# Optimization experiments

Measured on AMD Instinct MI355X. Metric: run time of the kernel, lower is better.

The kernel has to match this reference:

```python
import jax, jax.numpy as jnp
import numpy as np

# --- constants mirroring init_kwargs ---
DIM = 1024
N_HEADS = 16
N_KV_HEADS = 4
HEAD_DIM = DIM // N_HEADS          # 64
REP = N_HEADS // N_KV_HEADS        # 4
ROPE_THETA = 10000.0
WINDOW = 512
N_GLOBAL = 64
EPS = 1e-6


def setup_inputs() -> dict:
    key = jax.random.key(0)
    ks = jax.random.split(key, 7)
    B, L = 2, 2048
    x = jax.random.normal(ks[0], (B, L, DIM), dtype=jnp.float32)
    s = 0.02
    wq = jax.random.normal(ks[1], (DIM, N_HEADS * HEAD_DIM), dtype=jnp.float32) * s
    wk = jax.random.normal(ks[2], (DIM, N_KV_HEADS * HEAD_DIM), dtype=jnp.float32) * s
    wv = jax.random.normal(ks[3], (DIM, N_KV_HEADS * HEAD_DIM), dtype=jnp.float32) * s
    wo = jax.random.normal(ks[4], (N_HEADS * HEAD_DIM, DIM), dtype=jnp.float32) * s
    gq = jnp.ones((HEAD_DIM,), dtype=jnp.float32) + 0.01 * jax.random.normal(ks[5], (HEAD_DIM,), dtype=jnp.float32)
    gk = jnp.ones((HEAD_DIM,), dtype=jnp.float32) + 0.01 * jax.random.normal(ks[6], (HEAD_DIM,), dtype=jnp.float32)
    return {"x": x, "wq": wq, "wk": wk, "wv": wv, "wo": wo, "gq": gq, "gk": gk}


def _rmsnorm(t, g):
    # QKNorm: RMS norm over head_dim with learnable per-dim scale
    return t * jax.lax.rsqrt(jnp.mean(t * t, axis=-1, keepdims=True) + EPS) * g


def _rope(t, cos, sin):
    # t: [B,H,L,hd]; complex RoPE over consecutive pairs (2i, 2i+1)
    t1 = t[..., 0::2]
    t2 = t[..., 1::2]
    o1 = t1 * cos - t2 * sin
    o2 = t1 * sin + t2 * cos
    return jnp.stack([o1, o2], axis=-1).reshape(t.shape)


def reference(x, wq, wk, wv, wo, gq, gk):
    B, L, D = x.shape
    q = (x @ wq).reshape(B, L, N_HEADS, HEAD_DIM)
    k = (x @ wk).reshape(B, L, N_KV_HEADS, HEAD_DIM)
    v = (x @ wv).reshape(B, L, N_KV_HEADS, HEAD_DIM)
    q = _rmsnorm(q, gq)
    k = _rmsnorm(k, gk)
    q = q.transpose(0, 2, 1, 3)  # [B,H,L,hd]
    k = k.transpose(0, 2, 1, 3)
    v = v.transpose(0, 2, 1, 3)

    # RoPE frequencies (start_pos = 0)
    inv_freq = 1.0 / (ROPE_THETA ** (jnp.arange(0, HEAD_DIM, 2, dtype=jnp.float32) / HEAD_DIM))
    ang = jnp.arange(L, dtype=jnp.float32)[:, None] * inv_freq[None, :]  # [L, hd/2]
    cos, sin = jnp.cos(ang), jnp.sin(ang)
    q = _rope(q, cos, sin)
    k = _rope(k, cos, sin)

    # GQA: repeat kv heads (repeat_interleave on head dim)
    k = jnp.repeat(k, REP, axis=1)
    v = jnp.repeat(v, REP, axis=1)

    scores = jnp.einsum("bhqd,bhkd->bhqk", q, k) / np.sqrt(HEAD_DIM).astype(np.float32)

    # sliding-window + global-token causal mask
    half = WINDOW // 2
    i = jnp.arange(L)[:, None]
    j = jnp.arange(L)[None, :]
    m = (j <= i) & ((j >= i - half) | (j < N_GLOBAL))  # [L,L] bool
    scores = jnp.where(m[None, None], scores, -jnp.inf)

    attn = jax.nn.softmax(scores.astype(jnp.float32), axis=-1).astype(scores.dtype)
    out = jnp.einsum("bhqk,bhkd->bhqd", attn, v)
    out = out.transpose(0, 2, 1, 3).reshape(B, L, N_HEADS * HEAD_DIM)
    return out @ wo
```

## Files before the change

kernel.cpp:

```cpp
#include <hip/hip_runtime.h>
#include <hip/hip_bf16.h>

typedef __bf16 bf16x8 __attribute__((ext_vector_type(8)));
typedef __bf16 bf16x4 __attribute__((ext_vector_type(4)));
typedef float  f32x4  __attribute__((ext_vector_type(4)));
typedef short  s16x4  __attribute__((ext_vector_type(4)));

__device__ __forceinline__ __bf16 to_bf16(float f) {
    __hip_bfloat16 h = __float2bfloat16(f);
    return *reinterpret_cast<__bf16*>(&h);
}

__device__ __forceinline__ f32x4 mfma32(bf16x8 a, bf16x8 b, f32x4 c) {
    return __builtin_amdgcn_mfma_f32_16x16x32_bf16(a, b, c, 0, 0, 0);
}
__device__ __forceinline__ f32x4 mfma16(bf16x4 a, bf16x4 b, f32x4 c) {
#if __has_builtin(__builtin_amdgcn_mfma_f32_16x16x16_bf16)
    return __builtin_amdgcn_mfma_f32_16x16x16_bf16(a, b, c, 0, 0, 0);
#else
    return __builtin_amdgcn_mfma_f32_16x16x16bf16_1k(
        __builtin_bit_cast(s16x4, a), __builtin_bit_cast(s16x4, b), c, 0, 0, 0);
#endif
}

__device__ __forceinline__ void gload_lds16(const __bf16* g, __bf16* l) {
    __builtin_amdgcn_global_load_lds(
        (const __attribute__((address_space(1))) void*)g,
        (__attribute__((address_space(3))) void*)l, 16, 0, 0);
}


__global__ __launch_bounds__(256) void prep_k(const float* __restrict__ wq,
                                              const float* __restrict__ wk,
                                              const float* __restrict__ wv,
                                              __bf16* __restrict__ WqkvT,
                                              float2* __restrict__ rope_tab) {
    int b = blockIdx.x, tid = threadIdx.x;
    if (b >= 1536) {
        int idx = (b - 1536) * 256 + tid;
        int pos = idx >> 5, f = idx & 31;
        float ex = (float)(2 * f) * (1.0f / 64.0f);
        float invf = expf(-ex * 9.210340371976184f);
        float ang = (float)pos * invf;
        rope_tab[idx] = make_float2(cosf(ang), sinf(ang));
        return;
    }
    __shared__ float tile[32][36];
    const float* src; __bf16* dst; int N, idx;
    if (b < 1024)      { src = wq; dst = WqkvT;                        N = 1024; idx = b; }
    else if (b < 1280) { src = wk; dst = WqkvT + (size_t)1024 * 1024;  N = 256;  idx = b - 1024; }
    else               { src = wv; dst = WqkvT + (size_t)1280 * 1024;  N = 256;  idx = b - 1280; }
    int k0 = (idx & 31) * 32, n0 = (idx >> 5) * 32;
    int row = tid >> 3, c4 = tid & 7;
    *(f32x4*)&tile[row][c4 * 4] = *(const f32x4*)(src + (size_t)(k0 + row) * N + n0 + c4 * 4);
    __syncthreads();
    bf16x4 v;
#pragma unroll
    for (int j = 0; j < 4; ++j) v[j] = to_bf16(tile[c4 * 4 + j][row]);
    *(bf16x4*)&dst[(size_t)(n0 + row) * 1024 + k0 + c4 * 4] = v;
}

__global__ __launch_bounds__(512, 4) void gemmqkv_k(const float* __restrict__ X,
                                                    const __bf16* __restrict__ BT,
                                                    const float2* __restrict__ rope_tab,
                                                    const float* __restrict__ gq,
                                                    const float* __restrict__ gk,
                                                    const float* __restrict__ wo,
                                                    __bf16* __restrict__ Qb,
                                                    __bf16* __restrict__ Kbl,
                                                    __bf16* __restrict__ Vt,
                                                    __bf16* __restrict__ WoT) {
    extern __shared__ char smem_raw[];
    if (blockIdx.y >= 12) {
        float* scr = (float*)smem_raw;
        int bidT = (blockIdx.y - 12) * 32 + blockIdx.x;
        int sub = threadIdx.x >> 8, t8 = threadIdx.x & 255;
        int row = t8 >> 3, c4 = t8 & 7;
        float* my = scr + sub * 1152;
#pragma unroll
        for (int r = 0; r < 4; ++r) {
            int tile = bidT * 8 + r * 2 + sub;
            int k0 = (tile & 31) * 32, n0t = (tile >> 5) * 32;
            __syncthreads();
            *(f32x4*)&my[row * 36 + c4 * 4] =
                *(const f32x4*)(wo + (size_t)(k0 + row) * 1024 + n0t + c4 * 4);
            __syncthreads();
            bf16x4 v;
#pragma unroll
            for (int j = 0; j < 4; ++j) v[j] = to_bf16(my[(c4 * 4 + j) * 36 + row]);
            *(bf16x4*)&WoT[(size_t)(n0t + row) * 1024 + k0 + c4 * 4] = v;
        }
        return;
    }
    __shared__ float ssp[4][128];
    __bf16* smem = (__bf16*)smem_raw;
    int tid = threadIdx.x;
    int m0 = blockIdx.x * 128, n0 = blockIdx.y * 128;
    int wid = tid >> 6, lane = tid & 63;
    int wm = (wid & 1) * 64, wn = (wid >> 1) * 32;
    int lm = lane & 15, qd = lane >> 4;
    int srow = tid >> 2, sc4 = tid & 3;
    int ac16 = (tid & 3) * 16;
    int akh = ac16 >> 5, ac4 = (ac16 & 31) >> 3;
    f32x4 acc[4][2] = {};
    f32x4 areg[4];

    auto A_LOAD = [&](int t) {
        const float* ap = X + (size_t)(m0 + srow) * 1024 + t * 64 + ac16;
        areg[0] = *(const f32x4*)(ap);
        areg[1] = *(const f32x4*)(ap + 4);
        areg[2] = *(const f32x4*)(ap + 8);
        areg[3] = *(const f32x4*)(ap + 12);
    };
    auto A_WRITE = [&](int bsel) {
        __bf16* base = smem + bsel * 16384 + akh * 4096 + srow * 32;
        bf16x8 w0, w1;
#pragma unroll
        for (int j = 0; j < 4; ++j) {
            w0[j] = to_bf16(areg[0][j]); w0[4 + j] = to_bf16(areg[1][j]);
            w1[j] = to_bf16(areg[2][j]); w1[4 + j] = to_bf16(areg[3][j]);
        }
        *(bf16x8*)&base[ac4 * 8] = w0;
        *(bf16x8*)&base[(ac4 + 1) * 8] = w1;
    };
    auto B_GLOAD = [&](int bsel, int t) {
        __bf16* base = smem + bsel * 16384 + 8192;
#pragma unroll
        for (int kh = 0; kh < 2; ++kh)
            gload_lds16(BT + (size_t)(n0 + srow) * 1024 + t * 64 + kh * 32 + sc4 * 8,
                        base + kh * 4096 + wid * 512);
    };

    A_LOAD(0);
    B_GLOAD(0, 0);
    asm volatile("s_waitcnt vmcnt(2)" ::: "memory");
    A_WRITE(0);

    for (int t = 0; t < 16; ++t) {
        if (t + 1 < 16) {
            A_LOAD(t + 1);
            B_GLOAD((t + 1) & 1, t + 1);
            asm volatile("s_waitcnt vmcnt(6)" ::: "memory");
        } else {
            asm volatile("s_waitcnt vmcnt(0)" ::: "memory");
        }
        asm volatile("s_waitcnt lgkmcnt(0)" ::: "memory");
        __builtin_amdgcn_s_barrier();
        __builtin_amdgcn_sched_barrier(0);
        const __bf16* cA = smem + (t & 1) * 16384;
        const __bf16* cB = cA + 8192;
#pragma unroll
        for (int kh = 0; kh < 2; ++kh) {
            bf16x8 af[4], bfr[2];
#pragma unroll
            for (int t4 = 0; t4 < 4; ++t4) {
                int row = wm + t4 * 16 + lm;
                af[t4] = *(const bf16x8*)&cA[kh * 4096 + row * 32 + qd * 8];
            }
#pragma unroll
            for (int j = 0; j < 2; ++j) {
                int col = wn + j * 16 + lm;
                bfr[j] = *(const bf16x8*)&cB[kh * 4096 + col * 32 + qd * 8];
            }
#pragma unroll
            for (int ti = 0; ti < 4; ++ti)
#pragma unroll
                for (int tj = 0; tj < 2; ++tj)
                    acc[ti][tj] = mfma32(af[ti], bfr[tj], acc[ti][tj]);
        }
        if (t + 1 < 16) {
            asm volatile("s_waitcnt vmcnt(2)" ::: "memory");
            A_WRITE((t + 1) & 1);
        }
        asm volatile("s_waitcnt lgkmcnt(0)" ::: "memory");
        __builtin_amdgcn_s_barrier();
    }

    int head0 = n0 >> 6;
    int quad = wid >> 1;
    int chead = wn & 63;

    if (head0 < 20) {
        int head = head0 + (quad >> 1);
        bool isq = head < 16;
        const float* gvec = isq ? gq : gk;
        float gam[2];
#pragma unroll
        for (int tj = 0; tj < 2; ++tj) gam[tj] = gvec[chead + tj * 16 + lm];

#pragma unroll
        for (int ti = 0; ti < 4; ++ti)
#pragma unroll
            for (int r = 0; r < 4; ++r) {
                float sq = acc[ti][0][r] * acc[ti][0][r] + acc[ti][1][r] * acc[ti][1][r];
                sq += __shfl_xor(sq, 1);
                sq += __shfl_xor(sq, 2);
                sq += __shfl_xor(sq, 4);
                sq += __shfl_xor(sq, 8);
                if (lm == 0) ssp[quad][wm + ti * 16 + qd * 4 + r] = sq;
            }
        __syncthreads();

#pragma unroll
        for (int ti = 0; ti < 4; ++ti)
#pragma unroll
            for (int r = 0; r < 4; ++r) {
                int row = wm + ti * 16 + qd * 4 + r;
                int t = m0 + row;
                int pos = t & 2047, bb = t >> 11;
                float ss = ssp[quad][row] + ssp[quad ^ 1][row];
                float scale = rsqrtf(ss * (1.0f / 64.0f) + 1e-6f);
#pragma unroll
                for (int tj = 0; tj < 2; ++tj) {
                    int cw = chead + tj * 16 + lm;
                    float v = acc[ti][tj][r] * scale * gam[tj];
                    float2 cs = rope_tab[pos * 32 + (cw >> 1)];
                    float pv = __shfl_xor(v, 1);
                    float outv = (cw & 1) ? (pv * cs.y + v * cs.x) : (v * cs.x - pv * cs.y);
                    if (isq) {
                        int kvh = head >> 2, h4 = head & 3;
                        size_t off = (((((size_t)bb * 4 + kvh) * 128 + (pos >> 4)) * 4 + h4) * 16
                                      + (pos & 15)) * 64 + cw;
                        Qb[off] = to_bf16(outv * 0.125f);
                    } else {
                        int kvg = head - 16;
                        Kbl[(((size_t)bb * 4 + kvg) * 2048 + pos) * 64 + cw] = to_bf16(outv);
                    }
                }
            }
    } else {
        __bf16* tvh = smem + (quad >> 1) * 8704;
        int bb = m0 >> 11, pos0 = m0 & 2047;
#pragma unroll
        for (int ti = 0; ti < 4; ++ti)
#pragma unroll
            for (int tj = 0; tj < 2; ++tj)
#pragma unroll
                for (int r = 0; r < 4; ++r) {
                    int row = wm + ti * 16 + qd * 4 + r;
                    int cw = chead + tj * 16 + lm;
                    tvh[cw * 136 + row] = to_bf16(acc[ti][tj][r]);
                }
        __syncthreads();
        int hh = tid >> 8, t8 = tid & 255;
        int kvg = head0 + hh - 20;
        size_t gg = (size_t)bb * 4 + kvg;
        const __bf16* tvr = smem + hh * 8704;
#pragma unroll
        for (int p = 0; p < 4; ++p) {
            int d = p * 16 + (t8 >> 4);
            int tok = (t8 & 15) * 8;
            bf16x8 vvv = *(const bf16x8*)&tvr[d * 136 + tok];
            *(bf16x8*)(Vt + (gg * 64 + d) * 2048 + pos0 + tok) = vvv;
        }
    }
}

__global__ __launch_bounds__(512, 4) void gemm_op_k(const __bf16* __restrict__ A,
                                                    const __bf16* __restrict__ BT,
                                                    float* __restrict__ C) {
    extern __shared__ char smem_raw[];
    __bf16* smem = (__bf16*)smem_raw;
    int tid = threadIdx.x;
    int m0 = blockIdx.x * 128, n0 = blockIdx.y * 64;
    int wid = tid >> 6, lane = tid & 63;
    int wm = (wid & 3) * 32, wn = (wid >> 2) * 32;
    int lm = lane & 15, qd = lane >> 4;
    int srow = tid >> 2, sc4 = tid & 3;
    int bhalf = wid >> 2, bidx = tid & 255;
    int brow = bidx >> 2, bc4 = bidx & 3;
    f32x4 acc[2][2] = {};
    auto STAGE = [&](int bsel, int t) {
        __bf16* base = smem + bsel * 12288;
#pragma unroll
        for (int kh = 0; kh < 2; ++kh)
            gload_lds16(A + (size_t)(m0 + srow) * 1024 + t * 64 + kh * 32 + sc4 * 8,
                        base + kh * 4096 + wid * 512);
        gload_lds16(BT + (size_t)(n0 + brow) * 1024 + t * 64 + bhalf * 32 + bc4 * 8,
                    base + 8192 + bhalf * 2048 + (wid & 3) * 512);
    };
    STAGE(0, 0);
    for (int t = 0; t < 16; ++t) {
        if (t + 1 < 16) {
            STAGE((t + 1) & 1, t + 1);
            asm volatile("s_waitcnt vmcnt(3)" ::: "memory");
        } else {
            asm volatile("s_waitcnt vmcnt(0)" ::: "memory");
        }
        __builtin_amdgcn_s_barrier();
        __builtin_amdgcn_sched_barrier(0);
        const __bf16* cA = smem + (t & 1) * 12288;
        const __bf16* cB = cA + 8192;
#pragma unroll
        for (int kh = 0; kh < 2; ++kh) {
            bf16x8 af[2], bfr[2];
#pragma unroll
            for (int i = 0; i < 2; ++i) {
                int row = wm + i * 16 + lm;
                af[i] = *(const bf16x8*)&cA[kh * 4096 + row * 32 + qd * 8];
                int col = wn + i * 16 + lm;
                bfr[i] = *(const bf16x8*)&cB[kh * 2048 + col * 32 + qd * 8];
            }
#pragma unroll
            for (int ti = 0; ti < 2; ++ti)
#pragma unroll
                for (int tj = 0; tj < 2; ++tj)
                    acc[ti][tj] = mfma32(af[ti], bfr[tj], acc[ti][tj]);
        }
        asm volatile("s_waitcnt lgkmcnt(0)" ::: "memory");
        __builtin_amdgcn_s_barrier();
    }
#pragma unroll
    for (int ti = 0; ti < 2; ++ti)
#pragma unroll
        for (int tj = 0; tj < 2; ++tj)
#pragma unroll
            for (int r = 0; r < 4; ++r) {
                int row = m0 + wm + ti * 16 + qd * 4 + r;
                int col = n0 + wn + tj * 16 + lm;
                C[(size_t)row * 1024 + col] = acc[ti][tj][r];
            }
}

__global__ __launch_bounds__(512, 4) void attn_k(const __bf16* __restrict__ Qb,
                                                 const __bf16* __restrict__ Kbl,
                                                 const __bf16* __restrict__ Vt,
                                                 __bf16* __restrict__ aout) {
    __shared__ __bf16 Kt[2][64 * 64];
    __shared__ __bf16 Vl[2][64 * 64];
    int tid = threadIdx.x, wid = tid >> 6, lane = tid & 63;
    int l15 = lane & 15, quad = lane >> 4;
    int qb = blockIdx.x, kvh = blockIdx.y, b = blockIdx.z;
    int qg = wid >> 2;
    int h4 = wid & 3;
    int iw0 = qb * 32;
    int iw = iw0 + qg * 16;
    int g = b * 4 + kvh;
    int h = kvh * 4 + h4;
    int e7 = l15 & 7;

    int qbi = qb * 2 + qg;
    const __bf16* qp = Qb + ((((size_t)g * 128 + qbi) * 4 + h4) * 16 + l15) * 64 + quad * 8;
    bf16x8 qf0 = *(const bf16x8*)qp;
    bf16x8 qf1 = *(const bf16x8*)(qp + 32);

    int ts = (iw0 - 256) >> 6; if (ts < 1) ts = 1;
    int tmaxb = (iw0 + 31) >> 6;
    int n_all = (tmaxb >= ts) ? (tmaxb - ts + 2) : 1;
    int tmaxw = (iw + 15) >> 6;

    const __bf16* Kg = Kbl + (size_t)g * 2048 * 64;
    const __bf16* Vg = Vt + (size_t)g * 64 * 2048;

    int r0 = tid >> 3, c0 = tid & 7;
    int kl = r0 * 64 + ((c0 ^ (r0 & 7)) * 8);

    bf16x8 kr, vr;
    auto stage_load = [&](int tt) {
        kr = *(const bf16x8*)(Kg + (size_t)tt * 64 * 64 + r0 * 64 + c0 * 8);
        vr = *(const bf16x8*)(Vg + (size_t)r0 * 2048 + tt * 64 + c0 * 8);
    };
    auto stage_write = [&](int buf) {
        *(bf16x8*)&Kt[buf][kl] = kr;
        *(bf16x8*)&Vl[buf][kl] = vr;
    };

    stage_load(0);
    stage_write(0);

    f32x4 o[4] = {};
    float mr = -1e30f, lrp = 0.f;
    int iq = iw + l15;

    for (int idx = 0; idx < n_all; ++idx) {
        int tt = (idx == 0) ? 0 : ts + idx - 1;
        if (idx + 1 < n_all) stage_load(ts + idx);
        __syncthreads();
        int buf = idx & 1;

        f32x4 s[4] = {};
#pragma unroll
        for (int nt = 0; nt < 4; ++nt) {
            const __bf16* kp = &Kt[buf][(nt * 16 + l15) * 64];
            bf16x8 k0 = *(const bf16x8*)(kp + ((quad ^ e7) * 8));
            bf16x8 k1 = *(const bf16x8*)(kp + (((quad + 4) ^ e7) * 8));
            s[nt] = mfma32(k0, qf0, s[nt]);
            s[nt] = mfma32(k1, qf1, s[nt]);
        }

        bool need_mask = (tt >= tmaxw) || (tt >= 1 && tt * 64 < iw + 15 - 256);
        if (need_mask) {
#pragma unroll
            for (int nt = 0; nt < 4; ++nt)
#pragma unroll
                for (int r = 0; r < 4; ++r) {
                    int j = tt * 64 + nt * 16 + quad * 4 + r;
                    bool valid = (j <= iq) && ((j >= iq - 256) || (j < 64));
                    s[nt][r] = valid ? s[nt][r] : -1e30f;
                }
        }

        float mx = -1e30f;
#pragma unroll
        for (int nt = 0; nt < 4; ++nt)
#pragma unroll
            for (int r = 0; r < 4; ++r) mx = fmaxf(mx, s[nt][r]);
        mx = fmaxf(mx, __shfl_xor(mx, 16));
        mx = fmaxf(mx, __shfl_xor(mx, 32));
        float mn = fmaxf(mr, mx);
        float alpha = __expf(mr - mn);
        mr = mn;

        float ps = 0.f;
        bf16x4 pb[4];
#pragma unroll
        for (int nt = 0; nt < 4; ++nt)
#pragma unroll
            for (int r = 0; r < 4; ++r) {
                float pv = __expf(s[nt][r] - mn);
                ps += pv;
                pb[nt][r] = to_bf16(pv);
            }
        lrp = lrp * alpha + ps;

#pragma unroll
        for (int dt = 0; dt < 4; ++dt) {
            o[dt] *= alpha;
            const __bf16* vp = &Vl[buf][(dt * 16 + l15) * 64];
#pragma unroll
            for (int nt = 0; nt < 4; ++nt) {
                int c8 = 2 * nt + (quad >> 1);
                bf16x4 va = *(const bf16x4*)(vp + ((c8 ^ e7) * 8) + (quad & 1) * 4);
                o[dt] = mfma16(va, pb[nt], o[dt]);
            }
        }

        if (idx + 1 < n_all) stage_write((idx + 1) & 1);
    }

    lrp += __shfl_xor(lrp, 16);
    lrp += __shfl_xor(lrp, 32);
    float inv = 1.f / lrp;
    __syncthreads();
    __bf16* pr = (__bf16*)Kt + wid * 16 * 64;
#pragma unroll
    for (int dt = 0; dt < 4; ++dt)
#pragma unroll
        for (int r = 0; r < 4; ++r) {
            int e = dt * 16 + quad * 4 + r;
            int c8 = e >> 3;
            pr[l15 * 64 + ((c8 ^ e7) * 8) + (e & 7)] = to_bf16(o[dt][r] * inv);
        }
    bf16x8 o0 = *(const bf16x8*)(pr + l15 * 64 + (((2 * quad) ^ e7) * 8));
    bf16x8 o1 = *(const bf16x8*)(pr + l15 * 64 + (((2 * quad + 1) ^ e7) * 8));
    __bf16* op = aout + ((size_t)b * 2048 + iw + l15) * 1024 + h * 64 + quad * 16;
    *(bf16x8*)op = o0;
    *(bf16x8*)(op + 8) = o1;
}

extern "C" void kernel_launch(void* const* d_in, const int* in_sizes, int n_in,
                              void* d_out, int out_size, void* d_ws, size_t ws_size,
                              hipStream_t stream) {
    const float* x  = (const float*)d_in[0];
    const float* wq = (const float*)d_in[1];
    const float* wk = (const float*)d_in[2];
    const float* wv = (const float*)d_in[3];
    const float* wo = (const float*)d_in[4];
    const float* gq = (const float*)d_in[5];
    const float* gk = (const float*)d_in[6];
    float* out = (float*)d_out;

    char* ws = (char*)d_ws;
    __bf16*  WqkvT = (__bf16*)ws;
    __bf16*  WoT   = (__bf16*)(ws + 3145728);
    __bf16*  aout  = (__bf16*)(ws + 5242880);
    __bf16*  Kbl   = (__bf16*)(ws + 13631488);
    __bf16*  Vt    = (__bf16*)(ws + 15728640);
    __bf16*  Qb    = (__bf16*)(ws + 17825792);
    float2*  rtab  = (float2*)(ws + 26214400);

    prep_k<<<1792, dim3(256), 0, stream>>>(wq, wk, wv, WqkvT, rtab);
    gemmqkv_k<<<dim3(32, 16), dim3(512), 65536, stream>>>(x, WqkvT, rtab, gq, gk, wo,
                                                          Qb, Kbl, Vt, WoT);
    attn_k<<<dim3(64, 4, 2), dim3(512), 0, stream>>>(Qb, Kbl, Vt, aout);
    gemm_op_k<<<dim3(32, 16), dim3(512), 49152, stream>>>(aout, WoT, out);
}
```

Before: 142.1 us.

## Use 256-thread blocks with larger per-warp tiles in QKV and output GEMMs

Both GEMM kernels switch from 8 waves to 4 waves per block while keeping the same block tile, so each wave computes a bigger sub-tile (64x64 in QKV, 64x32 in the output projection). Each QKV wave now owns a full head's 64 columns, which lets the RMSNorm reduction run entirely with in-wave shuffles and drops the shared-memory partial-sum exchange and its barrier. The V transpose epilogue is serialized over two heads through one shared buffer. The aim is more MFMA work per LDS fragment load and less cross-wave synchronization, at the cost of more registers per thread and fewer waves to hide memory latency.

```diff
diff --git a/kernel.cpp b/kernel.cpp
--- a/kernel.cpp
+++ b/kernel.cpp
@@ -60,7 +60,7 @@
     *(bf16x4*)&dst[(size_t)(n0 + row) * 1024 + k0 + c4 * 4] = v;
 }
 
-__global__ __launch_bounds__(512, 4) void gemmqkv_k(const float* __restrict__ X,
+__global__ __launch_bounds__(256, 2) void gemmqkv_k(const float* __restrict__ X,
                                                     const __bf16* __restrict__ BT,
                                                     const float2* __restrict__ rope_tab,
                                                     const float* __restrict__ gq,
@@ -71,76 +71,76 @@
                                                     __bf16* __restrict__ Vt,
                                                     __bf16* __restrict__ WoT) {
     extern __shared__ char smem_raw[];
+    int tid = threadIdx.x;
     if (blockIdx.y >= 12) {
         float* scr = (float*)smem_raw;
         int bidT = (blockIdx.y - 12) * 32 + blockIdx.x;
-        int sub = threadIdx.x >> 8, t8 = threadIdx.x & 255;
-        int row = t8 >> 3, c4 = t8 & 7;
-        float* my = scr + sub * 1152;
-#pragma unroll
-        for (int r = 0; r < 4; ++r) {
-            int tile = bidT * 8 + r * 2 + sub;
+        int row = tid >> 3, c4 = tid & 7;
+#pragma unroll
+        for (int r = 0; r < 8; ++r) {
+            int tile = bidT * 8 + r;
             int k0 = (tile & 31) * 32, n0t = (tile >> 5) * 32;
             __syncthreads();
-            *(f32x4*)&my[row * 36 + c4 * 4] =
+            *(f32x4*)&scr[row * 36 + c4 * 4] =
                 *(const f32x4*)(wo + (size_t)(k0 + row) * 1024 + n0t + c4 * 4);
             __syncthreads();
             bf16x4 v;
 #pragma unroll
-            for (int j = 0; j < 4; ++j) v[j] = to_bf16(my[(c4 * 4 + j) * 36 + row]);
+            for (int j = 0; j < 4; ++j) v[j] = to_bf16(scr[(c4 * 4 + j) * 36 + row]);
             *(bf16x4*)&WoT[(size_t)(n0t + row) * 1024 + k0 + c4 * 4] = v;
         }
         return;
     }
-    __shared__ float ssp[4][128];
     __bf16* smem = (__bf16*)smem_raw;
-    int tid = threadIdx.x;
     int m0 = blockIdx.x * 128, n0 = blockIdx.y * 128;
     int wid = tid >> 6, lane = tid & 63;
-    int wm = (wid & 1) * 64, wn = (wid >> 1) * 32;
+    int wm = (wid & 1) * 64, wn = (wid >> 1) * 64;
     int lm = lane & 15, qd = lane >> 4;
-    int srow = tid >> 2, sc4 = tid & 3;
-    int ac16 = (tid & 3) * 16;
-    int akh = ac16 >> 5, ac4 = (ac16 & 31) >> 3;
-    f32x4 acc[4][2] = {};
-    f32x4 areg[4];
+    int srowA = tid >> 1, akh = tid & 1;
+    f32x4 acc[4][4] = {};
+    f32x4 areg[8];
 
     auto A_LOAD = [&](int t) {
-        const float* ap = X + (size_t)(m0 + srow) * 1024 + t * 64 + ac16;
-        areg[0] = *(const f32x4*)(ap);
-        areg[1] = *(const f32x4*)(ap + 4);
-        areg[2] = *(const f32x4*)(ap + 8);
-        areg[3] = *(const f32x4*)(ap + 12);
+        const float* ap = X + (size_t)(m0 + srowA) * 1024 + t * 64 + akh * 32;
+#pragma unroll
+        for (int j = 0; j < 8; ++j) areg[j] = *(const f32x4*)(ap + j * 4);
     };
     auto A_WRITE = [&](int bsel) {
-        __bf16* base = smem + bsel * 16384 + akh * 4096 + srow * 32;
-        bf16x8 w0, w1;
-#pragma unroll
-        for (int j = 0; j < 4; ++j) {
-            w0[j] = to_bf16(areg[0][j]); w0[4 + j] = to_bf16(areg[1][j]);
-            w1[j] = to_bf16(areg[2][j]); w1[4 + j] = to_bf16(areg[3][j]);
-        }
-        *(bf16x8*)&base[ac4 * 8] = w0;
-        *(bf16x8*)&base[(ac4 + 1) * 8] = w1;
+        __bf16* base = smem + bsel * 16384 + akh * 4096 + srowA * 32;
+#pragma unroll
+        for (int c8 = 0; c8 < 4; ++c8) {
+            bf16x8 w;
+#pragma unroll
+            for (int j = 0; j < 4; ++j) {
+                w[j] = to_bf16(areg[2 * c8][j]);
+                w[4 + j] = to_bf16(areg[2 * c8 + 1][j]);
+            }
+            *(bf16x8*)&base[c8 * 8] = w;
+        }
     };
     auto B_GLOAD = [&](int bsel, int t) {
         __bf16* base = smem + bsel * 16384 + 8192;
 #pragma unroll
         for (int kh = 0; kh < 2; ++kh)
-            gload_lds16(BT + (size_t)(n0 + srow) * 1024 + t * 64 + kh * 32 + sc4 * 8,
-                        base + kh * 4096 + wid * 512);
+#pragma unroll
+            for (int rr = 0; rr < 2; ++rr) {
+                int v = rr * 256 + tid;
+                int row = v >> 2, c4 = v & 3;
+                gload_lds16(BT + (size_t)(n0 + row) * 1024 + t * 64 + kh * 32 + c4 * 8,
+                            base + kh * 4096 + rr * 2048 + wid * 512);
+            }
     };
 
     A_LOAD(0);
     B_GLOAD(0, 0);
-    asm volatile("s_waitcnt vmcnt(2)" ::: "memory");
+    asm volatile("s_waitcnt vmcnt(4)" ::: "memory");
     A_WRITE(0);
 
     for (int t = 0; t < 16; ++t) {
         if (t + 1 < 16) {
             A_LOAD(t + 1);
             B_GLOAD((t + 1) & 1, t + 1);
-            asm volatile("s_waitcnt vmcnt(6)" ::: "memory");
+            asm volatile("s_waitcnt vmcnt(12)" ::: "memory");
         } else {
             asm volatile("s_waitcnt vmcnt(0)" ::: "memory");
         }
@@ -151,25 +151,20 @@
         const __bf16* cB = cA + 8192;
 #pragma unroll
         for (int kh = 0; kh < 2; ++kh) {
-            bf16x8 af[4], bfr[2];
+            bf16x8 af[4], bfr[4];
 #pragma unroll
             for (int t4 = 0; t4 < 4; ++t4) {
-                int row = wm + t4 * 16 + lm;
-                af[t4] = *(const bf16x8*)&cA[kh * 4096 + row * 32 + qd * 8];
-            }
-#pragma unroll
-            for (int j = 0; j < 2; ++j) {
-                int col = wn + j * 16 + lm;
-                bfr[j] = *(const bf16x8*)&cB[kh * 4096 + col * 32 + qd * 8];
+                af[t4] = *(const bf16x8*)&cA[kh * 4096 + (wm + t4 * 16 + lm) * 32 + qd * 8];
+                bfr[t4] = *(const bf16x8*)&cB[kh * 4096 + (wn + t4 * 16 + lm) * 32 + qd * 8];
             }
 #pragma unroll
             for (int ti = 0; ti < 4; ++ti)
 #pragma unroll
-                for (int tj = 0; tj < 2; ++tj)
+                for (int tj = 0; tj < 4; ++tj)
                     acc[ti][tj] = mfma32(af[ti], bfr[tj], acc[ti][tj]);
         }
         if (t + 1 < 16) {
-            asm volatile("s_waitcnt vmcnt(2)" ::: "memory");
+            asm volatile("s_waitcnt vmcnt(4)" ::: "memory");
             A_WRITE((t + 1) & 1);
         }
         asm volatile("s_waitcnt lgkmcnt(0)" ::: "memory");
@@ -177,30 +172,14 @@
     }
 
     int head0 = n0 >> 6;
-    int quad = wid >> 1;
-    int chead = wn & 63;
 
     if (head0 < 20) {
-        int head = head0 + (quad >> 1);
+        int head = head0 + (wn >> 6);
         bool isq = head < 16;
         const float* gvec = isq ? gq : gk;
-        float gam[2];
-#pragma unroll
-        for (int tj = 0; tj < 2; ++tj) gam[tj] = gvec[chead + tj * 16 + lm];
-
-#pragma unroll
-        for (int ti = 0; ti < 4; ++ti)
-#pragma unroll
-            for (int r = 0; r < 4; ++r) {
-                float sq = acc[ti][0][r] * acc[ti][0][r] + acc[ti][1][r] * acc[ti][1][r];
-                sq += __shfl_xor(sq, 1);
-                sq += __shfl_xor(sq, 2);
-                sq += __shfl_xor(sq, 4);
-                sq += __shfl_xor(sq, 8);
-                if (lm == 0) ssp[quad][wm + ti * 16 + qd * 4 + r] = sq;
-            }
-        __syncthreads();
-
+        float gam[4];
+#pragma unroll
+        for (int tj = 0; tj < 4; ++tj) gam[tj] = gvec[tj * 16 + lm];
 #pragma unroll
         for (int ti = 0; ti < 4; ++ti)
 #pragma unroll
@@ -208,11 +187,16 @@
                 int row = wm + ti * 16 + qd * 4 + r;
                 int t = m0 + row;
                 int pos = t & 2047, bb = t >> 11;
-                float ss = ssp[quad][row] + ssp[quad ^ 1][row];
+                float ss = acc[ti][0][r] * acc[ti][0][r] + acc[ti][1][r] * acc[ti][1][r]
+                         + acc[ti][2][r] * acc[ti][2][r] + acc[ti][3][r] * acc[ti][3][r];
+                ss += __shfl_xor(ss, 1);
+                ss += __shfl_xor(ss, 2);
+                ss += __shfl_xor(ss, 4);
+                ss += __shfl_xor(ss, 8);
                 float scale = rsqrtf(ss * (1.0f / 64.0f) + 1e-6f);
 #pragma unroll
-                for (int tj = 0; tj < 2; ++tj) {
-                    int cw = chead + tj * 16 + lm;
+                for (int tj = 0; tj < 4; ++tj) {
+                    int cw = tj * 16 + lm;
                     float v = acc[ti][tj][r] * scale * gam[tj];
                     float2 cs = rope_tab[pos * 32 + (cw >> 1)];
                     float pv = __shfl_xor(v, 1);
@@ -229,34 +213,38 @@
                 }
             }
     } else {
-        __bf16* tvh = smem + (quad >> 1) * 8704;
+        __bf16* tv = smem;
         int bb = m0 >> 11, pos0 = m0 & 2047;
 #pragma unroll
-        for (int ti = 0; ti < 4; ++ti)
-#pragma unroll
-            for (int tj = 0; tj < 2; ++tj)
-#pragma unroll
-                for (int r = 0; r < 4; ++r) {
-                    int row = wm + ti * 16 + qd * 4 + r;
-                    int cw = chead + tj * 16 + lm;
-                    tvh[cw * 136 + row] = to_bf16(acc[ti][tj][r]);
-                }
-        __syncthreads();
-        int hh = tid >> 8, t8 = tid & 255;
-        int kvg = head0 + hh - 20;
-        size_t gg = (size_t)bb * 4 + kvg;
-        const __bf16* tvr = smem + hh * 8704;
-#pragma unroll
-        for (int p = 0; p < 4; ++p) {
-            int d = p * 16 + (t8 >> 4);
-            int tok = (t8 & 15) * 8;
-            bf16x8 vvv = *(const bf16x8*)&tvr[d * 136 + tok];
-            *(bf16x8*)(Vt + (gg * 64 + d) * 2048 + pos0 + tok) = vvv;
-        }
-    }
-}
-
-__global__ __launch_bounds__(512, 4) void gemm_op_k(const __bf16* __restrict__ A,
+        for (int hh = 0; hh < 2; ++hh) {
+            if ((wn >> 6) == hh) {
+#pragma unroll
+                for (int ti = 0; ti < 4; ++ti)
+#pragma unroll
+                    for (int tj = 0; tj < 4; ++tj)
+#pragma unroll
+                        for (int r = 0; r < 4; ++r) {
+                            int row = wm + ti * 16 + qd * 4 + r;
+                            int cw = tj * 16 + lm;
+                            tv[cw * 136 + row] = to_bf16(acc[ti][tj][r]);
+                        }
+            }
+            __syncthreads();
+            int kvg = head0 + hh - 20;
+            size_t gg = (size_t)bb * 4 + kvg;
+#pragma unroll
+            for (int p = 0; p < 4; ++p) {
+                int d = p * 16 + (tid >> 4);
+                int tok = (tid & 15) * 8;
+                bf16x8 vvv = *(const bf16x8*)&tv[d * 136 + tok];
+                *(bf16x8*)(Vt + (gg * 64 + d) * 2048 + pos0 + tok) = vvv;
+            }
+            __syncthreads();
+        }
+    }
+}
+
+__global__ __launch_bounds__(256, 2) void gemm_op_k(const __bf16* __restrict__ A,
                                                     const __bf16* __restrict__ BT,
                                                     float* __restrict__ C) {
     extern __shared__ char smem_raw[];
@@ -264,26 +252,31 @@
     int tid = threadIdx.x;
     int m0 = blockIdx.x * 128, n0 = blockIdx.y * 64;
     int wid = tid >> 6, lane = tid & 63;
-    int wm = (wid & 3) * 32, wn = (wid >> 2) * 32;
+    int wm = (wid & 1) * 64, wn = (wid >> 1) * 32;
     int lm = lane & 15, qd = lane >> 4;
-    int srow = tid >> 2, sc4 = tid & 3;
-    int bhalf = wid >> 2, bidx = tid & 255;
-    int brow = bidx >> 2, bc4 = bidx & 3;
-    f32x4 acc[2][2] = {};
+    int brow = tid >> 2, bc4 = tid & 3;
+    f32x4 acc[4][2] = {};
     auto STAGE = [&](int bsel, int t) {
         __bf16* base = smem + bsel * 12288;
 #pragma unroll
         for (int kh = 0; kh < 2; ++kh)
-            gload_lds16(A + (size_t)(m0 + srow) * 1024 + t * 64 + kh * 32 + sc4 * 8,
-                        base + kh * 4096 + wid * 512);
-        gload_lds16(BT + (size_t)(n0 + brow) * 1024 + t * 64 + bhalf * 32 + bc4 * 8,
-                    base + 8192 + bhalf * 2048 + (wid & 3) * 512);
+#pragma unroll
+            for (int rr = 0; rr < 2; ++rr) {
+                int v = rr * 256 + tid;
+                int row = v >> 2, c4 = v & 3;
+                gload_lds16(A + (size_t)(m0 + row) * 1024 + t * 64 + kh * 32 + c4 * 8,
+                            base + kh * 4096 + rr * 2048 + wid * 512);
+            }
+#pragma unroll
+        for (int kh = 0; kh < 2; ++kh)
+            gload_lds16(BT + (size_t)(n0 + brow) * 1024 + t * 64 + kh * 32 + bc4 * 8,
+                        base + 8192 + kh * 2048 + wid * 512);
     };
     STAGE(0, 0);
     for (int t = 0; t < 16; ++t) {
         if (t + 1 < 16) {
             STAGE((t + 1) & 1, t + 1);
-            asm volatile("s_waitcnt vmcnt(3)" ::: "memory");
+            asm volatile("s_waitcnt vmcnt(6)" ::: "memory");
         } else {
             asm volatile("s_waitcnt vmcnt(0)" ::: "memory");
         }
@@ -293,16 +286,15 @@
         const __bf16* cB = cA + 8192;
 #pragma unroll
         for (int kh = 0; kh < 2; ++kh) {
-            bf16x8 af[2], bfr[2];
-#pragma unroll
-            for (int i = 0; i < 2; ++i) {
-                int row = wm + i * 16 + lm;
-                af[i] = *(const bf16x8*)&cA[kh * 4096 + row * 32 + qd * 8];
-                int col = wn + i * 16 + lm;
-                bfr[i] = *(const bf16x8*)&cB[kh * 2048 + col * 32 + qd * 8];
-            }
-#pragma unroll
-            for (int ti = 0; ti < 2; ++ti)
+            bf16x8 af[4], bfr[2];
+#pragma unroll
+            for (int t4 = 0; t4 < 4; ++t4)
+                af[t4] = *(const bf16x8*)&cA[kh * 4096 + (wm + t4 * 16 + lm) * 32 + qd * 8];
+#pragma unroll
+            for (int j = 0; j < 2; ++j)
+                bfr[j] = *(const bf16x8*)&cB[kh * 2048 + (wn + j * 16 + lm) * 32 + qd * 8];
+#pragma unroll
+            for (int ti = 0; ti < 4; ++ti)
 #pragma unroll
                 for (int tj = 0; tj < 2; ++tj)
                     acc[ti][tj] = mfma32(af[ti], bfr[tj], acc[ti][tj]);
@@ -311,7 +303,7 @@
         __builtin_amdgcn_s_barrier();
     }
 #pragma unroll
-    for (int ti = 0; ti < 2; ++ti)
+    for (int ti = 0; ti < 4; ++ti)
 #pragma unroll
         for (int tj = 0; tj < 2; ++tj)
 #pragma unroll
@@ -480,8 +472,8 @@
     float2*  rtab  = (float2*)(ws + 26214400);
 
     prep_k<<<1792, dim3(256), 0, stream>>>(wq, wk, wv, WqkvT, rtab);
-    gemmqkv_k<<<dim3(32, 16), dim3(512), 65536, stream>>>(x, WqkvT, rtab, gq, gk, wo,
+    gemmqkv_k<<<dim3(32, 16), dim3(256), 65536, stream>>>(x, WqkvT, rtab, gq, gk, wo,
                                                           Qb, Kbl, Vt, WoT);
     attn_k<<<dim3(64, 4, 2), dim3(512), 0, stream>>>(Qb, Kbl, Vt, aout);
-    gemm_op_k<<<dim3(32, 16), dim3(512), 49152, stream>>>(aout, WoT, out);
-}
+    gemm_op_k<<<dim3(32, 16), dim3(256), 49152, stream>>>(aout, WoT, out);
+}
```

New measurement: 153.8 us. 1.08x slower.
